# Kernel tuning notes

Hardware: AMD Instinct MI355X
Metric: run time of the kernel (lower is better)

Reference implementation:

```python
import jax, jax.numpy as jnp
import numpy as np

B, C = 4096, 16384
SCALE = 16.0
MARGIN = 0.1
NEG_INF = -10000.0
HARD_SCALE = 1.0 + 0.012
HARD_SHIFT = 0.012


def setup_inputs() -> dict:
    key = jax.random.key(0)
    k1, k2, k3 = jax.random.split(key, 3)
    inputs = jax.random.normal(k1, (B, C), dtype=jnp.float32)
    targets = jax.random.randint(k2, (B,), 0, C, dtype=jnp.int64)
    # camera-positive mask: 0/1 floats
    pos_cam_mask = jax.random.bernoulli(k3, 0.5, (B, C)).astype(jnp.float32)
    mask = jnp.zeros((B, C), dtype=bool)  # unused by the module (overwritten)
    return {"inputs": inputs, "targets": targets, "mask": mask, "pos_cam_mask": pos_cam_mask}


def reference(inputs, targets, mask, pos_cam_mask):
    b, c = inputs.shape
    rows = jnp.arange(b)
    one_hot = jax.nn.one_hot(targets, c, dtype=inputs.dtype)  # (B, C)
    # camera-masked logits; non-positive-cam entries pushed to -10000
    cam_inputs = pos_cam_mask * inputs + (1.0 - pos_cam_mask) * NEG_INF
    gt = inputs[rows, targets]  # (B,) target logit, pre-modification
    hard_mask = cam_inputs >= gt[:, None]  # (B, C)
    # rescale hard examples: x <- 1.012 * x + 0.012 where hard
    x = jnp.where(hard_mask, HARD_SCALE * inputs + HARD_SHIFT, inputs)
    # restore original gt logit at target positions (scatter_)
    x = jnp.where(one_hot > 0, gt[:, None], x)
    output = SCALE * (x - one_hot * MARGIN)
    # mean cross-entropy
    logp = jax.nn.log_softmax(output, axis=-1)
    loss = -jnp.mean(logp[rows, targets])
    return loss
```

## Files before the change

kernel.cpp:

```cpp
#include <hip/hip_runtime.h>


#define B_ 4096
#define C_ 16384
#define LOG2E 1.44269504088896340736f

__global__ __launch_bounds__(256, 4) void coscam_loss_kernel(
    const float* __restrict__ inputs,
    const int*   __restrict__ targets,
    const float* __restrict__ pos_mask,
    float*       __restrict__ out)
{
    const int row = blockIdx.x;
    const int tid = threadIdx.x;

    __shared__ float s_gt;
    __shared__ int   s_t;
    __shared__ float red_s[4];

    if (tid == 0) {
        int t = targets[row];
        s_t  = t;
        s_gt = inputs[(size_t)row * C_ + t];
    }
    __syncthreads();

    const float gt    = s_gt;
    const int   t     = s_t;
    const float wt    = gt - 0.1f;
    const float out_t = 16.0f * wt;
    const float shift = fmaxf(out_t, 40.0f);
    const float nshift2 = -shift * LOG2E;
    const float k16l2e = 16.0f * LOG2E;

    const float* __restrict__ rin = inputs   + (size_t)row * C_;
    const float* __restrict__ rpm = pos_mask + (size_t)row * C_;

    float acc0 = 0.0f, acc1 = 0.0f, acc2 = 0.0f, acc3 = 0.0f;

    #pragma unroll 4
    for (int c = tid * 4; c < C_; c += 256 * 4) {
        const float4 x4 = *(const float4*)(rin + c);
        const float4 p4 = *(const float4*)(rpm + c);

        float w0 = ((p4.x > 0.5f) && (x4.x >= gt)) ? fmaf(1.012f, x4.x, 0.012f) : x4.x;
        float w1 = ((p4.y > 0.5f) && (x4.y >= gt)) ? fmaf(1.012f, x4.y, 0.012f) : x4.y;
        float w2 = ((p4.z > 0.5f) && (x4.z >= gt)) ? fmaf(1.012f, x4.z, 0.012f) : x4.z;
        float w3 = ((p4.w > 0.5f) && (x4.w >= gt)) ? fmaf(1.012f, x4.w, 0.012f) : x4.w;

        w0 = (c + 0 == t) ? wt : w0;
        w1 = (c + 1 == t) ? wt : w1;
        w2 = (c + 2 == t) ? wt : w2;
        w3 = (c + 3 == t) ? wt : w3;

        acc0 += __builtin_amdgcn_exp2f(fmaf(w0, k16l2e, nshift2));
        acc1 += __builtin_amdgcn_exp2f(fmaf(w1, k16l2e, nshift2));
        acc2 += __builtin_amdgcn_exp2f(fmaf(w2, k16l2e, nshift2));
        acc3 += __builtin_amdgcn_exp2f(fmaf(w3, k16l2e, nshift2));
    }

    float s = (acc0 + acc1) + (acc2 + acc3);

    #pragma unroll
    for (int off = 32; off > 0; off >>= 1)
        s += __shfl_down(s, off);

    const int wave = tid >> 6;
    const int lane = tid & 63;
    if (lane == 0) red_s[wave] = s;
    __syncthreads();

    if (tid == 0) {
        const float total = (red_s[0] + red_s[1]) + (red_s[2] + red_s[3]);
        const float loss_row = (__logf(total) + shift) - out_t;
        atomicAdd(out, loss_row * (1.0f / (float)B_));
    }
}

extern "C" void kernel_launch(void* const* d_in, const int* in_sizes, int n_in,
                              void* d_out, int out_size, void* d_ws, size_t ws_size,
                              hipStream_t stream) {
    const float* inputs   = (const float*)d_in[0];
    const int*   targets  = (const int*)  d_in[1];
    const float* pos_mask = (const float*)d_in[3];
    float* out = (float*)d_out;

    (void)hipMemsetAsync(out, 0, sizeof(float), stream);

    coscam_loss_kernel<<<dim3(B_), dim3(256), 0, stream>>>(inputs, targets, pos_mask, out);
}
```

Before: 597.6 us.

## Issue all row loads up front and correct target term after reduction

Each thread now issues all 16 float4 loads of inputs and mask into registers before computing, which raises memory-level parallelism. The per-element target check is removed, and the target column's contribution is fixed once at the end by adding the correct term and subtracting the one computed in the loop. The shared-memory broadcast and the barrier at the start are replaced by each thread loading the target and gt directly. The cost is heavy register use (128 VGPRs of loads), lower occupancy (launch bounds 4 to 3), and a cancellation step that can lose float precision.

```diff
diff --git a/kernel.cpp b/kernel.cpp
--- a/kernel.cpp
+++ b/kernel.cpp
@@ -5,7 +5,7 @@
 #define C_ 16384
 #define LOG2E 1.44269504088896340736f
 
-__global__ __launch_bounds__(256, 4) void coscam_loss_kernel(
+__global__ __launch_bounds__(256, 3) void coscam_loss_kernel(
     const float* __restrict__ inputs,
     const int*   __restrict__ targets,
     const float* __restrict__ pos_mask,
@@ -14,45 +14,36 @@
     const int row = blockIdx.x;
     const int tid = threadIdx.x;
 
-    __shared__ float s_gt;
-    __shared__ int   s_t;
-    __shared__ float red_s[4];
-
-    if (tid == 0) {
-        int t = targets[row];
-        s_t  = t;
-        s_gt = inputs[(size_t)row * C_ + t];
-    }
-    __syncthreads();
-
-    const float gt    = s_gt;
-    const int   t     = s_t;
-    const float wt    = gt - 0.1f;
-    const float out_t = 16.0f * wt;
-    const float shift = fmaxf(out_t, 40.0f);
-    const float nshift2 = -shift * LOG2E;
-    const float k16l2e = 16.0f * LOG2E;
-
     const float* __restrict__ rin = inputs   + (size_t)row * C_;
     const float* __restrict__ rpm = pos_mask + (size_t)row * C_;
 
+    const int   t     = targets[row];
+    const float gt    = rin[t];
+    const float pos_t = rpm[t];
+
+    const float wt      = gt - 0.1f;
+    const float out_t   = 16.0f * wt;
+    const float shift   = fmaxf(out_t, 40.0f);
+    const float nshift2 = -shift * LOG2E;
+    const float k16l2e  = 16.0f * LOG2E;
+
+    float4 xs[16], ps[16];
+    #pragma unroll
+    for (int u = 0; u < 16; ++u) {
+        const int c = u * 1024 + tid * 4;
+        xs[u] = *(const float4*)(rin + c);
+        ps[u] = *(const float4*)(rpm + c);
+    }
+
     float acc0 = 0.0f, acc1 = 0.0f, acc2 = 0.0f, acc3 = 0.0f;
-
-    #pragma unroll 4
-    for (int c = tid * 4; c < C_; c += 256 * 4) {
-        const float4 x4 = *(const float4*)(rin + c);
-        const float4 p4 = *(const float4*)(rpm + c);
-
-        float w0 = ((p4.x > 0.5f) && (x4.x >= gt)) ? fmaf(1.012f, x4.x, 0.012f) : x4.x;
-        float w1 = ((p4.y > 0.5f) && (x4.y >= gt)) ? fmaf(1.012f, x4.y, 0.012f) : x4.y;
-        float w2 = ((p4.z > 0.5f) && (x4.z >= gt)) ? fmaf(1.012f, x4.z, 0.012f) : x4.z;
-        float w3 = ((p4.w > 0.5f) && (x4.w >= gt)) ? fmaf(1.012f, x4.w, 0.012f) : x4.w;
-
-        w0 = (c + 0 == t) ? wt : w0;
-        w1 = (c + 1 == t) ? wt : w1;
-        w2 = (c + 2 == t) ? wt : w2;
-        w3 = (c + 3 == t) ? wt : w3;
-
+    #pragma unroll
+    for (int u = 0; u < 16; ++u) {
+        const float4 x4 = xs[u];
+        const float4 p4 = ps[u];
+        const float w0 = ((p4.x > 0.5f) && (x4.x >= gt)) ? fmaf(1.012f, x4.x, 0.012f) : x4.x;
+        const float w1 = ((p4.y > 0.5f) && (x4.y >= gt)) ? fmaf(1.012f, x4.y, 0.012f) : x4.y;
+        const float w2 = ((p4.z > 0.5f) && (x4.z >= gt)) ? fmaf(1.012f, x4.z, 0.012f) : x4.z;
+        const float w3 = ((p4.w > 0.5f) && (x4.w >= gt)) ? fmaf(1.012f, x4.w, 0.012f) : x4.w;
         acc0 += __builtin_amdgcn_exp2f(fmaf(w0, k16l2e, nshift2));
         acc1 += __builtin_amdgcn_exp2f(fmaf(w1, k16l2e, nshift2));
         acc2 += __builtin_amdgcn_exp2f(fmaf(w2, k16l2e, nshift2));
@@ -65,13 +56,17 @@
     for (int off = 32; off > 0; off >>= 1)
         s += __shfl_down(s, off);
 
+    __shared__ float red_s[4];
     const int wave = tid >> 6;
     const int lane = tid & 63;
     if (lane == 0) red_s[wave] = s;
     __syncthreads();
 
     if (tid == 0) {
-        const float total = (red_s[0] + red_s[1]) + (red_s[2] + red_s[3]);
+        float total = (red_s[0] + red_s[1]) + (red_s[2] + red_s[3]);
+        const float w_wrong = (pos_t > 0.5f) ? fmaf(1.012f, gt, 0.012f) : gt;
+        total += __builtin_amdgcn_exp2f(fmaf(wt,      k16l2e, nshift2))
+               - __builtin_amdgcn_exp2f(fmaf(w_wrong, k16l2e, nshift2));
         const float loss_row = (__logf(total) + shift) - out_t;
         atomicAdd(out, loss_row * (1.0f / (float)B_));
     }
```

After: 597.4 us. About the same (-0.0%).
